# Kernel optimization log

Hardware: AMD Instinct MI355X
Metric: run time of the kernel (lower is better)

The kernel has to match this reference:

```python
import jax, jax.numpy as jnp
import numpy as np

B, Q, M, H, D = 2, 2048, 2048, 16, 64
HID = H * D           # hidden_size == num_heads * head_size
K_LEN = M + Q         # key/value length after memory concat
EPS = 1e-3            # keras LayerNormalization default epsilon
RAMP = 32             # Adaptive_Span ramp_size
NEG = -1e9


def setup_inputs() -> dict:
    key = jax.random.key(0)
    ks = jax.random.split(key, 12)
    s = 0.02
    return {
        "query": jax.random.normal(ks[0], (B, Q, HID), jnp.float32),
        "memory": jax.random.normal(ks[1], (B, M, HID), jnp.float32),
        "Wq": jax.random.normal(ks[2], (HID, H * D), jnp.float32) * s,
        "Wk": jax.random.normal(ks[3], (HID, H * D), jnp.float32) * s,
        "Wv": jax.random.normal(ks[4], (HID, H * D), jnp.float32) * s,
        "Wo": jax.random.normal(ks[5], (H * D, HID), jnp.float32) * s,
        "Wr": jax.random.normal(ks[6], (HID, H * D), jnp.float32) * s,
        "gamma_mem": jnp.ones((HID,), jnp.float32),
        "beta_mem": jnp.zeros((HID,), jnp.float32),
        "gamma_q": jnp.ones((HID,), jnp.float32),
        "beta_q": jnp.zeros((HID,), jnp.float32),
        "r_w_bias": jax.random.normal(ks[7], (1, H, 1, D), jnp.float32) * s,
        "r_r_bias": jax.random.normal(ks[8], (1, H, 1, D), jnp.float32) * s,
        "span_val": jnp.zeros((1, H, 1, 1), jnp.float32),
    }


def _layer_norm(x, gamma, beta):
    mu = jnp.mean(x, axis=-1, keepdims=True)
    var = jnp.mean(jnp.square(x - mu), axis=-1, keepdims=True)
    return (x - mu) * jax.lax.rsqrt(var + EPS) * gamma + beta


def _rel_shift(x):
    # Transformer-XL relative shift on [B,H,Q,K]
    b, h, q, k = x.shape
    x = jnp.pad(x, ((0, 0), (0, 0), (0, 0), (1, 0)))
    x = x.reshape(b, h, k + 1, q)[:, :, 1:, :]
    return x.reshape(b, h, q, k)


def reference(query, memory, Wq, Wk, Wv, Wo, Wr,
              gamma_mem, beta_mem, gamma_q, beta_q,
              r_w_bias, r_r_bias, span_val):
    kv = jnp.concatenate([memory, query], axis=1)          # [B,K,HID]
    kv = _layer_norm(kv, gamma_mem, beta_mem)
    q_in = _layer_norm(query, gamma_q, beta_q)

    # sinusoidal relative position embedding, positions K-1 .. 0
    pos_seq = jnp.arange(K_LEN - 1, -1, -1, dtype=jnp.float32)
    inv_freq = 1.0 / (10000.0 ** (jnp.arange(0, HID, 2, dtype=jnp.float32) / HID))
    sin_inp = pos_seq[:, None] * inv_freq[None, :]
    pos_emb = jnp.concatenate([jnp.sin(sin_inp), jnp.cos(sin_inp)], axis=-1)  # [K,HID]

    q = (q_in @ Wq).reshape(B, Q, H, D).transpose(0, 2, 1, 3)      # [B,H,Q,D]
    k = (kv @ Wk).reshape(B, K_LEN, H, D).transpose(0, 2, 1, 3)    # [B,H,K,D]
    v = (kv @ Wv).reshape(B, K_LEN, H, D).transpose(0, 2, 1, 3)    # [B,H,K,D]
    rel = (pos_emb @ Wr).reshape(K_LEN, H, D).transpose(1, 0, 2)   # [H,K,D]

    AD = jnp.einsum('bhqd,bhkd->bhqk', q + r_w_bias, k)
    BD = _rel_shift(jnp.einsum('bhqd,hkd->bhqk', q + r_r_bias, rel))
    logits = (AD + BD) / D                                          # note: /head_size, not sqrt

    # causal bias over the query block, zeros over memory columns
    causal = jnp.triu(jnp.ones((Q, Q), jnp.float32), 1) * NEG
    bias = jnp.concatenate([jnp.zeros((Q, M), jnp.float32), causal], axis=-1)
    logits = logits + bias[None, None]

    w = jax.nn.softmax(logits, axis=-1)                             # [B,H,Q,K]

    # adaptive span masking (static current_val path)
    mt = jnp.arange(Q, dtype=jnp.float32)
    span_mask = jnp.clip((mt[None, None, None, :] + span_val * Q) / (RAMP + 1), 0.0, 1.0)
    full_mask = jnp.concatenate(
        [jnp.ones((1, H, 1, M), jnp.float32),
         jnp.broadcast_to(span_mask, (1, H, 1, Q))], axis=-1)       # [1,H,1,K]
    w = w * full_mask
    w = w / (jnp.sum(w, axis=-1, keepdims=True) + 1e-8)

    out = jnp.einsum('bhqk,bhkd->bhqd', w, v)
    out = out.transpose(0, 2, 1, 3).reshape(B, Q, H * D)
    return out @ Wo
```

## Files before the change

### kernel.cpp

```cpp
#include <hip/hip_runtime.h>
#include <hip/hip_bf16.h>
#include <math.h>

#define B_   2
#define Q_   2048
#define M_   2048
#define H_   16
#define D_   64
#define HID_ 1024
#define KL_  4096
#define RT_  128
#define WT_  64
#define LSCL 0.022542110013890053f

typedef short short8 __attribute__((ext_vector_type(8)));
typedef short short4v __attribute__((ext_vector_type(4)));
typedef float f32x4 __attribute__((ext_vector_type(4)));
typedef float f32x16 __attribute__((ext_vector_type(16)));
typedef unsigned int uint2v __attribute__((ext_vector_type(2)));

__device__ __forceinline__ void async_copy16(const void* g, void* l) {
  __builtin_amdgcn_global_load_lds((const __attribute__((address_space(1))) unsigned int*)g,
                                   (__attribute__((address_space(3))) unsigned int*)l,
                                   16, 0, 0);
}

__device__ __forceinline__ float ldin(const void* p, size_t i, int md) {
  return md ? ((const float*)p)[i] : __bfloat162float(((const __hip_bfloat16*)p)[i]);
}

__device__ __forceinline__ short bfbits(float v) {
  __hip_bfloat16 t = __float2bfloat16(v);
  return *(short*)&t;
}

__device__ __forceinline__ float fexp2(float x) { return exp2f(x); }

__global__ __launch_bounds__(256) void detect_kernel(const unsigned int* __restrict__ q,
                                                     int* __restrict__ flag) {
  __shared__ int cnt;
  if (threadIdx.x == 0) cnt = 0;
  __syncthreads();
  int ins = 0;
#pragma unroll
  for (int i = 0; i < 4; i++) {
    unsigned int u = q[threadIdx.x * 4 + i];
    int e0 = (int)((u >> 7) & 0xffu);
    int e1 = (int)((u >> 23) & 0xffu);
    if (e0 == 0xff || e0 < 102 || e0 > 140) ins++;
    if (e1 == 0xff || e1 < 102 || e1 > 140) ins++;
  }
  atomicAdd(&cnt, ins);
  __syncthreads();
  if (threadIdx.x == 0) *flag = (cnt > 512) ? 1 : 0;
}

__global__ __launch_bounds__(256) void wtpe_kernel(
    const void* __restrict__ s0, const void* __restrict__ s1, const void* __restrict__ s2,
    const void* __restrict__ s3, const void* __restrict__ s4,
    __hip_bfloat16* __restrict__ d0, __hip_bfloat16* __restrict__ d1,
    __hip_bfloat16* __restrict__ d2, __hip_bfloat16* __restrict__ d3,
    __hip_bfloat16* __restrict__ d4, __hip_bfloat16* __restrict__ pe,
    const int* __restrict__ mode) {
  const int tid = threadIdx.x;
  if (blockIdx.z >= 5) {
    const int p = (blockIdx.z - 5) * 256 + blockIdx.y * 16 + blockIdx.x;
    const float pos = (float)(KL_ - 1 - p);
#pragma unroll
    for (int i = 0; i < 4; i++) {
      int c = tid * 4 + i;
      int f = (c < 512) ? c : c - 512;
      float invf = fexp2(-(float)f * (13.287712379549449f / 512.0f));
      float a = pos * invf;
      float v = (c < 512) ? __sinf(a) : __cosf(a);
      pe[(size_t)p * HID_ + c] = __float2bfloat16(v);
    }
    return;
  }
  const int md = *mode;
  const void* src; __hip_bfloat16* dst;
  switch (blockIdx.z) {
    case 0: src = s0; dst = d0; break;
    case 1: src = s1; dst = d1; break;
    case 2: src = s2; dst = d2; break;
    case 3: src = s3; dst = d3; break;
    default: src = s4; dst = d4; break;
  }
  const int r0 = blockIdx.x * 64, c0 = blockIdx.y * 64;
  __shared__ __hip_bfloat16 t[64][65];
  const int col = tid & 63, r4 = tid >> 6;
#pragma unroll
  for (int i = 0; i < 16; i++)
    t[r4 + i * 4][col] = __float2bfloat16(ldin(src, (size_t)(r0 + r4 + i * 4) * HID_ + c0 + col, md));
  __syncthreads();
#pragma unroll
  for (int i = 0; i < 16; i++)
    dst[(size_t)(c0 + r4 + i * 4) * HID_ + r0 + col] = t[col][r4 + i * 4];
}

__global__ __launch_bounds__(256) void ln_kernel(
    const void* __restrict__ mem, const void* __restrict__ qry,
    const void* __restrict__ gmem, const void* __restrict__ bmem,
    const void* __restrict__ gq, const void* __restrict__ bq,
    __hip_bfloat16* __restrict__ kvout, __hip_bfloat16* __restrict__ qout,
    const int* __restrict__ mode) {
  const int md = *mode;
  const int row = blockIdx.x;
  const void* src;
  const void* gamma; const void* beta;
  size_t base;
  __hip_bfloat16* dst;
  if (row < B_ * KL_) {
    const int b = row / KL_, j = row % KL_;
    if (j < M_) { src = mem; base = ((size_t)b * M_ + j) * HID_; }
    else        { src = qry; base = ((size_t)b * Q_ + (j - M_)) * HID_; }
    gamma = gmem; beta = bmem;
    dst = kvout + (size_t)row * HID_;
  } else {
    const int r = row - B_ * KL_;
    src = qry; base = (size_t)r * HID_;
    gamma = gq; beta = bq;
    dst = qout + (size_t)r * HID_;
  }
  const int tid = threadIdx.x;
  float x[4];
  float s = 0.f, ss = 0.f;
#pragma unroll
  for (int i = 0; i < 4; i++) {
    x[i] = ldin(src, base + i * 256 + tid, md);
    s += x[i]; ss += x[i] * x[i];
  }
#pragma unroll
  for (int o = 32; o > 0; o >>= 1) { s += __shfl_down(s, o); ss += __shfl_down(ss, o); }
  __shared__ float red[8];
  if ((tid & 63) == 0) { red[(tid >> 6) * 2] = s; red[(tid >> 6) * 2 + 1] = ss; }
  __syncthreads();
  float ts = 0.f, tss = 0.f;
#pragma unroll
  for (int i = 0; i < 4; i++) { ts += red[i * 2]; tss += red[i * 2 + 1]; }
  const float mu = ts * (1.f / 1024.f);
  const float var = tss * (1.f / 1024.f) - mu * mu;
  const float rs = rsqrtf(var + 1e-3f);
#pragma unroll
  for (int i = 0; i < 4; i++) {
    int c = i * 256 + tid;
    dst[c] = __float2bfloat16((x[i] - mu) * rs * ldin(gamma, c, md) + ldin(beta, c, md));
  }
}

template <int WRITE_MODE_SWITCH>
__device__ __forceinline__ void gemm_body(const __hip_bfloat16* __restrict__ A,
                                          const __hip_bfloat16* __restrict__ BT,
                                          void* __restrict__ C, int md, float scl) {
  __shared__ __attribute__((aligned(16))) __hip_bfloat16 sA[128 * 64];
  __shared__ __attribute__((aligned(16))) __hip_bfloat16 sB[128 * 64];
  const int tid = threadIdx.x;
  const int lane = tid & 63;
  const int w = tid >> 6;
  const int quad = lane >> 4, l16 = lane & 15;
  const int m0 = blockIdx.x * 128;
  const int n0 = blockIdx.y * 128;
  const int wm = (w >> 1) * 64, wn = (w & 1) * 64;
  const f32x4 fz = {0.f, 0.f, 0.f, 0.f};

  f32x4 acc[4][4];
#pragma unroll
  for (int i = 0; i < 4; i++)
#pragma unroll
    for (int j = 0; j < 4; j++) acc[i][j] = fz;

  for (int kk = 0; kk < HID_ / 64; kk++) {
    const int k0 = kk * 64;
    __syncthreads();
#pragma unroll
    for (int t = 0; t < 4; t++) {
      int c = (w * 4 + t) * 64 + lane;
      int row = c >> 3;
      int cid = (c & 7) ^ (row & 7);
      async_copy16(A + (size_t)(m0 + row) * HID_ + k0 + cid * 8, (char*)sA + c * 16);
      async_copy16(BT + (size_t)(n0 + row) * HID_ + k0 + cid * 8, (char*)sB + c * 16);
    }
    __syncthreads();
#pragma unroll
    for (int half = 0; half < 2; half++) {
      short8 af[4], bf[4];
#pragma unroll
      for (int mt = 0; mt < 4; mt++) {
        int r = wm + mt * 16 + l16;
        af[mt] = *(const short8*)((const char*)sA + r * 128 + (((half * 4 + quad) ^ (r & 7)) * 16));
      }
#pragma unroll
      for (int nt = 0; nt < 4; nt++) {
        int r = wn + nt * 16 + l16;
        bf[nt] = *(const short8*)((const char*)sB + r * 128 + (((half * 4 + quad) ^ (r & 7)) * 16));
      }
#pragma unroll
      for (int mt = 0; mt < 4; mt++)
#pragma unroll
        for (int nt = 0; nt < 4; nt++)
          acc[mt][nt] = __builtin_amdgcn_mfma_f32_16x16x32_bf16(af[mt], bf[nt], acc[mt][nt], 0, 0, 0);
    }
  }
#pragma unroll
  for (int mt = 0; mt < 4; mt++)
#pragma unroll
    for (int nt = 0; nt < 4; nt++)
#pragma unroll
      for (int rg = 0; rg < 4; rg++) {
        int r = m0 + wm + mt * 16 + quad * 4 + rg;
        int cc = n0 + wn + nt * 16 + l16;
        size_t idx = (size_t)r * HID_ + cc;
        if (WRITE_MODE_SWITCH && md) ((float*)C)[idx] = acc[mt][nt][rg];
        else ((__hip_bfloat16*)C)[idx] = __float2bfloat16(acc[mt][nt][rg] * scl);
      }
}

__global__ __launch_bounds__(256) void gemm_bt128(const __hip_bfloat16* __restrict__ A,
                                                  const __hip_bfloat16* __restrict__ BT,
                                                  __hip_bfloat16* __restrict__ C, float scl) {
  gemm_body<0>(A, BT, (void*)C, 0, scl);
}

__global__ __launch_bounds__(256) void gemm_out(const __hip_bfloat16* __restrict__ A,
                                                const __hip_bfloat16* __restrict__ BT,
                                                void* __restrict__ C,
                                                const int* __restrict__ mode) {
  gemm_body<1>(A, BT, C, *mode, 1.0f);
}

__global__ __launch_bounds__(256) void gemm_q(const __hip_bfloat16* __restrict__ A,
                                              const __hip_bfloat16* __restrict__ BT,
                                              const void* __restrict__ rwb,
                                              const void* __restrict__ rrb,
                                              __hip_bfloat16* __restrict__ qw,
                                              __hip_bfloat16* __restrict__ qr,
                                              const int* __restrict__ mode) {
  const int md = *mode;
  __shared__ __attribute__((aligned(16))) __hip_bfloat16 sA[128 * 64];
  __shared__ __attribute__((aligned(16))) __hip_bfloat16 sB[128 * 64];
  const int tid = threadIdx.x;
  const int lane = tid & 63;
  const int w = tid >> 6;
  const int quad = lane >> 4, l16 = lane & 15;
  const int m0 = blockIdx.x * 128;
  const int n0 = blockIdx.y * 128;
  const int wm = (w >> 1) * 64, wn = (w & 1) * 64;
  const f32x4 fz = {0.f, 0.f, 0.f, 0.f};

  f32x4 acc[4][4];
#pragma unroll
  for (int i = 0; i < 4; i++)
#pragma unroll
    for (int j = 0; j < 4; j++) acc[i][j] = fz;

  for (int kk = 0; kk < HID_ / 64; kk++) {
    const int k0 = kk * 64;
    __syncthreads();
#pragma unroll
    for (int t = 0; t < 4; t++) {
      int c = (w * 4 + t) * 64 + lane;
      int row = c >> 3;
      int cid = (c & 7) ^ (row & 7);
      async_copy16(A + (size_t)(m0 + row) * HID_ + k0 + cid * 8, (char*)sA + c * 16);
      async_copy16(BT + (size_t)(n0 + row) * HID_ + k0 + cid * 8, (char*)sB + c * 16);
    }
    __syncthreads();
#pragma unroll
    for (int half = 0; half < 2; half++) {
      short8 af[4], bf[4];
#pragma unroll
      for (int mt = 0; mt < 4; mt++) {
        int r = wm + mt * 16 + l16;
        af[mt] = *(const short8*)((const char*)sA + r * 128 + (((half * 4 + quad) ^ (r & 7)) * 16));
      }
#pragma unroll
      for (int nt = 0; nt < 4; nt++) {
        int r = wn + nt * 16 + l16;
        bf[nt] = *(const short8*)((const char*)sB + r * 128 + (((half * 4 + quad) ^ (r & 7)) * 16));
      }
#pragma unroll
      for (int mt = 0; mt < 4; mt++)
#pragma unroll
        for (int nt = 0; nt < 4; nt++)
          acc[mt][nt] = __builtin_amdgcn_mfma_f32_16x16x32_bf16(af[mt], bf[nt], acc[mt][nt], 0, 0, 0);
    }
  }
  float bw[4], br[4];
#pragma unroll
  for (int nt = 0; nt < 4; nt++) {
    int cc = n0 + wn + nt * 16 + l16;
    bw[nt] = ldin(rwb, cc, md);
    br[nt] = ldin(rrb, cc, md);
  }
#pragma unroll
  for (int mt = 0; mt < 4; mt++)
#pragma unroll
    for (int nt = 0; nt < 4; nt++)
#pragma unroll
      for (int rg = 0; rg < 4; rg++) {
        int r = m0 + wm + mt * 16 + quad * 4 + rg;
        int cc = n0 + wn + nt * 16 + l16;
        size_t idx = (size_t)r * HID_ + cc;
        float a = acc[mt][nt][rg];
        qw[idx] = __float2bfloat16((a + bw[nt]) * LSCL);
        qr[idx] = __float2bfloat16((a + br[nt]) * LSCL);
      }
}

__global__ __launch_bounds__(256) void gemm_dualv(const __hip_bfloat16* __restrict__ A,
                                                  const __hip_bfloat16* __restrict__ BT,
                                                  __hip_bfloat16* __restrict__ C0,
                                                  __hip_bfloat16* __restrict__ vpt) {
  __shared__ __attribute__((aligned(16))) char smem[128 * 136 * 2];
  __hip_bfloat16* sA = (__hip_bfloat16*)smem;
  __hip_bfloat16* sB = (__hip_bfloat16*)(smem + 16384);
  short* sT = (short*)smem;
  const int tid = threadIdx.x;
  const int lane = tid & 63;
  const int w = tid >> 6;
  const int quad = lane >> 4, l16 = lane & 15;
  const int m0 = blockIdx.x * 128;
  const int n0 = blockIdx.y * 128;
  const int wm = (w >> 1) * 64, wn = (w & 1) * 64;
  const f32x4 fz = {0.f, 0.f, 0.f, 0.f};

  f32x4 acc[4][4];
#pragma unroll
  for (int i = 0; i < 4; i++)
#pragma unroll
    for (int j = 0; j < 4; j++) acc[i][j] = fz;

  for (int kk = 0; kk < HID_ / 64; kk++) {
    const int k0 = kk * 64;
    __syncthreads();
#pragma unroll
    for (int t = 0; t < 4; t++) {
      int c = (w * 4 + t) * 64 + lane;
      int row = c >> 3;
      int cid = (c & 7) ^ (row & 7);
      async_copy16(A + (size_t)(m0 + row) * HID_ + k0 + cid * 8, (char*)sA + c * 16);
      async_copy16(BT + (size_t)(n0 + row) * HID_ + k0 + cid * 8, (char*)sB + c * 16);
    }
    __syncthreads();
#pragma unroll
    for (int half = 0; half < 2; half++) {
      short8 af[4], bf[4];
#pragma unroll
      for (int mt = 0; mt < 4; mt++) {
        int r = wm + mt * 16 + l16;
        af[mt] = *(const short8*)((const char*)sA + r * 128 + (((half * 4 + quad) ^ (r & 7)) * 16));
      }
#pragma unroll
      for (int nt = 0; nt < 4; nt++) {
        int r = wn + nt * 16 + l16;
        bf[nt] = *(const short8*)((const char*)sB + r * 128 + (((half * 4 + quad) ^ (r & 7)) * 16));
      }
#pragma unroll
      for (int mt = 0; mt < 4; mt++)
#pragma unroll
        for (int nt = 0; nt < 4; nt++)
          acc[mt][nt] = __builtin_amdgcn_mfma_f32_16x16x32_bf16(af[mt], bf[nt], acc[mt][nt], 0, 0, 0);
    }
  }
  if (n0 < HID_) {
#pragma unroll
    for (int mt = 0; mt < 4; mt++)
#pragma unroll
      for (int nt = 0; nt < 4; nt++)
#pragma unroll
        for (int rg = 0; rg < 4; rg++) {
          int r = m0 + wm + mt * 16 + quad * 4 + rg;
          int cc = n0 + wn + nt * 16 + l16;
          C0[(size_t)r * HID_ + cc] = __float2bfloat16(acc[mt][nt][rg]);
        }
  } else {
    __syncthreads();
#pragma unroll
    for (int mt = 0; mt < 4; mt++)
#pragma unroll
      for (int nt = 0; nt < 4; nt++) {
        int r = wm + mt * 16 + quad * 4;
        int cc = wn + nt * 16 + l16;
        short4v pk;
#pragma unroll
        for (int rg = 0; rg < 4; rg++) pk[rg] = bfbits(acc[mt][nt][rg]);
        *(short4v*)&sT[cc * 136 + r] = pk;
      }
    __syncthreads();
    const int b = m0 >> 12;
    const int j0g = m0 & (KL_ - 1);
    const int cg0 = n0 - HID_;
#pragma unroll
    for (int it = 0; it < 16; it++) {
      int cc = it * 8 + w * 2 + (lane >> 5);
      int jj = (lane & 31) * 4;
      int cg = cg0 + cc;
      int h = cg >> 6, d = cg & 63;
      short4v v = *(const short4v*)&sT[cc * 136 + jj];
      *(short4v*)(vpt + (((size_t)(b * H_ + h)) * D_ + d) * KL_ + j0g + jj) = v;
    }
  }
}

__global__ __launch_bounds__(256, 2) void attn_kernel(
    const __hip_bfloat16* __restrict__ qpw, const __hip_bfloat16* __restrict__ qpr,
    const __hip_bfloat16* __restrict__ kp, const __hip_bfloat16* __restrict__ vpt,
    const __hip_bfloat16* __restrict__ relp,
    const void* __restrict__ spanv, __hip_bfloat16* __restrict__ attn_out,
    const int* __restrict__ mode) {
  const int md = *mode;
  const int bid = blockIdx.x;
  int rk = (bid >> 3) & 15;
  if (bid & 256) rk ^= 15;
  const int i0 = rk << 7;
  const int bh = (bid & 7) + 8 * (bid >> 7);
  const int b = bh >> 4, h = bh & 15;

  const int tid = threadIdx.x;
  const int lane = tid & 63;
  const int w = tid >> 6;
  const int l31 = lane & 31, hi = lane >> 5;
  const int di = w * 32 + l31;
  const int iRow = i0 + di;

  __shared__ __attribute__((aligned(16))) __hip_bfloat16 sk[64 * 64];
  __shared__ __attribute__((aligned(16))) __hip_bfloat16 srel[192 * 64];
  __shared__ __attribute__((aligned(16))) __hip_bfloat16 svt[64 * 64];
  __shared__ __attribute__((aligned(16))) short sTP[128 * 100];

  const int rb = di * 200;
  const int sw = l31 & 7;

  const __hip_bfloat16* kbase = kp + (size_t)b * KL_ * HID_ + h * D_;
  const __hip_bfloat16* vtb = vpt + ((size_t)(b * H_ + h)) * D_ * KL_;
  const float sv = ldin(spanv, h, md);
  const float svQ = sv * (float)Q_;
  const int pb0 = Q_ - RT_ - i0;
  const int wof = (3 - w) * 32;
  const int ntiles = ((M_ + i0 + RT_ - 1) >> 6) + 1;

  const f32x16 z16 = {0.f,0.f,0.f,0.f,0.f,0.f,0.f,0.f,0.f,0.f,0.f,0.f,0.f,0.f,0.f,0.f};

  short8 qf[4], qrf[4];
  {
    const size_t qofs = ((size_t)(b * Q_ + iRow)) * HID_ + h * D_;
#pragma unroll
    for (int ks = 0; ks < 4; ks++) {
      qf[ks]  = *(const short8*)(qpw + qofs + ks * 16 + hi * 8);
      qrf[ks] = *(const short8*)(qpr + qofs + ks * 16 + hi * 8);
    }
  }

  {
#pragma unroll
    for (int t = 0; t < 2; t++) {
      int c = (w * 2 + t) * 64 + lane;
      int row = c >> 3;
      int cid = (c & 7) ^ (row & 7);
      async_copy16(kbase + (size_t)row * HID_ + cid * 8, (char*)sk + c * 16);
      async_copy16(vtb + (size_t)row * KL_ + cid * 8, (char*)svt + c * 16);
    }
#pragma unroll
    for (int t = 0; t < 6; t++) {
      int c = (w * 6 + t) * 64 + lane;
      int row = c >> 3;
      int cid = (c & 7) ^ (row & 7);
      int p = pb0 + row; p = p < KL_ ? p : KL_ - 1;
      async_copy16(relp + (size_t)p * HID_ + h * D_ + cid * 8, (char*)srel + c * 16);
    }
  }

  float mrow = -3e38f, lrow = 0.f, dfrow = 0.f;
  f32x16 oacc[2];
  oacc[0] = z16; oacc[1] = z16;
  int rot = 0;

  for (int kt = 0; kt < ntiles; kt++) {
    const int j0 = kt * WT_;

    __syncthreads();

    short8 rK[2], rR[2], rV[2];
    const bool pf = (kt + 1 < ntiles);
    {
      int j0n = j0 + WT_; if (j0n > KL_ - WT_) j0n = KL_ - WT_;
#pragma unroll
      for (int t = 0; t < 2; t++) {
        int c = (w * 2 + t) * 64 + lane;
        int row = c >> 3;
        int cid = (c & 7) ^ (row & 7);
        rK[t] = *(const short8*)(kbase + (size_t)(j0n + row) * HID_ + cid * 8);
        rV[t] = *(const short8*)(vtb + (size_t)row * KL_ + j0n + cid * 8);
        int p = pb0 + (kt + 1) * 64 + 128 + row; p = p < KL_ ? p : KL_ - 1;
        rR[t] = *(const short8*)(relp + (size_t)p * HID_ + h * D_ + cid * 8);
      }
    }
    __builtin_amdgcn_sched_barrier(0);

    __builtin_amdgcn_s_setprio(1);
    f32x16 S[2];
    S[0] = z16; S[1] = z16;
#pragma unroll
    for (int mt = 0; mt < 2; mt++) {
      const char* rowp = (const char*)sk + (mt * 32 + l31) * 128;
#pragma unroll
      for (int ks = 0; ks < 4; ks++) {
        short8 af = *(const short8*)(rowp + (((ks * 2 + hi) ^ sw) * 16));
        S[mt] = __builtin_amdgcn_mfma_f32_32x32x16_bf16(af, qf[ks], S[mt], 0, 0, 0);
      }
    }

#pragma unroll
    for (int mt = 0; mt < 3; mt++) {
      f32x16 T = z16;
      int rr = wof + mt * 32 + l31 + rot; if (rr >= 192) rr -= 192;
      const char* rowp = (const char*)srel + rr * 128;
#pragma unroll
      for (int ks = 0; ks < 4; ks++) {
        short8 af = *(const short8*)(rowp + (((ks * 2 + hi) ^ sw) * 16));
        T = __builtin_amdgcn_mfma_f32_32x32x16_bf16(af, qrf[ks], T, 0, 0, 0);
      }
#pragma unroll
      for (int r2 = 0; r2 < 4; r2++) {
        short4v pk;
#pragma unroll
        for (int r4 = 0; r4 < 4; r4++) pk[r4] = bfbits(T[r2 * 4 + r4]);
        *(short4v*)((char*)sTP + rb + (mt * 32 + 8 * r2 + 4 * hi) * 2) = pk;
      }
    }
    __builtin_amdgcn_s_setprio(0);

    {
      const char* tb2 = (const char*)sTP + rb + (31 - l31 + 4 * hi) * 2;
#pragma unroll
      for (int mt = 0; mt < 2; mt++)
#pragma unroll
        for (int r2 = 0; r2 < 4; r2++)
#pragma unroll
          for (int r4 = 0; r4 < 4; r4++)
            S[mt][r2 * 4 + r4] +=
                __bfloat162float(*(const __hip_bfloat16*)(tb2 + (mt * 32 + 8 * r2 + r4) * 2));
    }

    const bool causalT = (j0 + WT_ - 1 - i0) > M_;
    if (causalT) {
#pragma unroll
      for (int mt = 0; mt < 2; mt++)
#pragma unroll
        for (int r2 = 0; r2 < 4; r2++)
#pragma unroll
          for (int r4 = 0; r4 < 4; r4++) {
            int j = j0 + mt * 32 + 8 * r2 + 4 * hi + r4;
            if (j - iRow > M_) S[mt][r2 * 4 + r4] = -1e30f;
          }
    }
    float m8[8];
#pragma unroll
    for (int g = 0; g < 8; g++) {
      int mt = g >> 2, r2 = g & 3;
      m8[g] = fmaxf(fmaxf(S[mt][r2 * 4 + 0], S[mt][r2 * 4 + 1]),
                    fmaxf(S[mt][r2 * 4 + 2], S[mt][r2 * 4 + 3]));
    }
    float mnew = fmaxf(mrow,
        fmaxf(fmaxf(fmaxf(m8[0], m8[1]), fmaxf(m8[2], m8[3])),
              fmaxf(fmaxf(m8[4], m8[5]), fmaxf(m8[6], m8[7]))));
    mnew = fmaxf(mnew, __shfl_xor(mnew, 32));
    if (!__all(mnew - mrow <= 8.f)) {
      const float alpha = fexp2(mrow - mnew);
      mrow = mnew;
      lrow *= alpha; dfrow *= alpha;
#pragma unroll
      for (int dt = 0; dt < 2; dt++)
#pragma unroll
        for (int rg = 0; rg < 16; rg++) oacc[dt][rg] *= alpha;
    }

    const bool maskT = (j0 + WT_ > M_) && ((float)j0 < (float)M_ + 33.f - svQ);
    short8 paf[4];
#pragma unroll
    for (int mt = 0; mt < 2; mt++) {
      unsigned Pp[4][2];
#pragma unroll
      for (int r2 = 0; r2 < 4; r2++) {
        short4v g;
        float pvv[4];
#pragma unroll
        for (int r4 = 0; r4 < 4; r4++) {
          float pv = fexp2(S[mt][r2 * 4 + r4] - mrow);
          pvv[r4] = pv;
          float pm = pv;
          if (maskT) {
            int j = j0 + mt * 32 + 8 * r2 + 4 * hi + r4;
            if (j >= M_) {
              float t0 = (float)(j - M_) + svQ;
              float mk = fminf(fmaxf(t0 * (1.0f / 33.0f), 0.f), 1.f);
              pm = pv * mk;
              dfrow += pv - pm;
            }
          }
          g[r4] = bfbits(pm);
        }
        lrow += (pvv[0] + pvv[1]) + (pvv[2] + pvv[3]);
        union { short4v s; unsigned u[2]; } cv; cv.s = g;
        Pp[r2][0] = cv.u[0]; Pp[r2][1] = cv.u[1];
      }
#pragma unroll
      for (int half = 0; half < 2; half++) {
        uint2v rA = __builtin_amdgcn_permlane32_swap(Pp[half * 2][0], Pp[half * 2 + 1][0], false, false);
        uint2v rB = __builtin_amdgcn_permlane32_swap(Pp[half * 2][1], Pp[half * 2 + 1][1], false, false);
        union { unsigned u[4]; short8 s; } asm8;
        asm8.u[0] = rA[0]; asm8.u[1] = rB[0]; asm8.u[2] = rA[1]; asm8.u[3] = rB[1];
        paf[mt * 2 + half] = asm8.s;
      }
    }

    __builtin_amdgcn_s_setprio(1);
#pragma unroll
    for (int dt = 0; dt < 2; dt++) {
      const char* rowp = (const char*)svt + (dt * 32 + l31) * 128;
#pragma unroll
      for (int ks = 0; ks < 4; ks++) {
        short8 bfv = *(const short8*)(rowp + (((ks * 2 + hi) ^ sw) * 16));
        oacc[dt] = __builtin_amdgcn_mfma_f32_32x32x16_bf16(bfv, paf[ks], oacc[dt], 0, 0, 0);
      }
    }
    __builtin_amdgcn_s_setprio(0);

    __syncthreads();

    if (pf) {
#pragma unroll
      for (int t = 0; t < 2; t++) {
        int c = (w * 2 + t) * 64 + lane;
        int row = c >> 3;
        *(short8*)((char*)sk + c * 16) = rK[t];
        *(short8*)((char*)svt + c * 16) = rV[t];
        *(short8*)((char*)srel + (rot + row) * 128 + (c & 7) * 16) = rR[t];
      }
    }
    rot += 64; if (rot == 192) rot = 0;
  }

  lrow += __shfl_xor(lrow, 32);
  dfrow += __shfl_xor(dfrow, 32);
  const float denom = (lrow - dfrow) + 1e-8f * lrow;
  const float rdenom = 1.f / denom;
  __hip_bfloat16* ob = attn_out + ((size_t)(b * Q_ + iRow)) * HID_ + h * D_;
#pragma unroll
  for (int dt = 0; dt < 2; dt++)
#pragma unroll
    for (int r2 = 0; r2 < 4; r2++) {
      short4v o;
#pragma unroll
      for (int r4 = 0; r4 < 4; r4++) o[r4] = bfbits(oacc[dt][r2 * 4 + r4] * rdenom);
      *(short4v*)(ob + dt * 32 + 8 * r2 + 4 * hi) = o;
    }
}

extern "C" void kernel_launch(void* const* d_in, const int* in_sizes, int n_in,
                              void* d_out, int out_size, void* d_ws, size_t ws_size,
                              hipStream_t stream) {
  const void* query  = d_in[0];
  const void* memory = d_in[1];
  const void* Wq = d_in[2];
  const void* Wk = d_in[3];
  const void* Wv = d_in[4];
  const void* Wo = d_in[5];
  const void* Wr = d_in[6];
  const void* gmem = d_in[7];
  const void* bmem = d_in[8];
  const void* gq = d_in[9];
  const void* bq = d_in[10];
  const void* rwb = d_in[11];
  const void* rrb = d_in[12];
  const void* spanv = d_in[13];

  char* ws = (char*)d_ws;
  size_t off = 0;
  auto alloc = [&](size_t bytes) -> char* {
    char* p = ws + off;
    off += (bytes + 255) & ~(size_t)255;
    return p;
  };
  int* flag = (int*)alloc(256);
  const size_t SZ_W = (size_t)HID_ * HID_ * 2;
  __hip_bfloat16* wqT = (__hip_bfloat16*)alloc(SZ_W);
  __hip_bfloat16* wkT = (__hip_bfloat16*)alloc(SZ_W);
  __hip_bfloat16* wvT = (__hip_bfloat16*)alloc(SZ_W);
  __hip_bfloat16* wrT = (__hip_bfloat16*)alloc(SZ_W);
  __hip_bfloat16* woT = (__hip_bfloat16*)alloc(SZ_W);
  __hip_bfloat16* kvln = (__hip_bfloat16*)alloc((size_t)B_ * KL_ * HID_ * 2);
  __hip_bfloat16* qln  = (__hip_bfloat16*)alloc((size_t)B_ * Q_ * HID_ * 2);
  __hip_bfloat16* pe   = (__hip_bfloat16*)alloc((size_t)KL_ * HID_ * 2);
  __hip_bfloat16* qpw  = (__hip_bfloat16*)alloc((size_t)B_ * Q_ * HID_ * 2);
  __hip_bfloat16* qpr  = (__hip_bfloat16*)alloc((size_t)B_ * Q_ * HID_ * 2);
  __hip_bfloat16* kpb  = (__hip_bfloat16*)alloc((size_t)B_ * KL_ * HID_ * 2);
  __hip_bfloat16* vptb = (__hip_bfloat16*)alloc((size_t)B_ * KL_ * HID_ * 2);
  __hip_bfloat16* relp = (__hip_bfloat16*)alloc((size_t)KL_ * HID_ * 2);
  __hip_bfloat16* aout = (__hip_bfloat16*)alloc((size_t)B_ * Q_ * HID_ * 2);

  dim3 tb(256);
  detect_kernel<<<dim3(1), tb, 0, stream>>>((const unsigned int*)query, flag);

  wtpe_kernel<<<dim3(16, 16, 21), tb, 0, stream>>>(Wq, Wk, Wv, Wr, Wo,
                                                   wqT, wkT, wvT, wrT, woT, pe, flag);

  ln_kernel<<<dim3(B_ * KL_ + B_ * Q_), tb, 0, stream>>>(memory, query, gmem, bmem, gq, bq,
                                                         kvln, qln, flag);

  gemm_q<<<dim3(B_ * Q_ / 128, HID_ / 128), tb, 0, stream>>>(qln, wqT, rwb, rrb, qpw, qpr, flag);
  gemm_dualv<<<dim3(B_ * KL_ / 128, 2 * HID_ / 128), tb, 0, stream>>>(kvln, wkT, kpb, vptb);
  gemm_bt128<<<dim3(KL_ / 128, HID_ / 128), tb, 0, stream>>>(pe, wrT, relp, 1.0f);

  attn_kernel<<<dim3((Q_ / RT_) * H_ * B_), tb, 0, stream>>>(qpw, qpr, kpb, vptb, relp, spanv, aout, flag);

  gemm_out<<<dim3(B_ * Q_ / 128, HID_ / 128), tb, 0, stream>>>(aout, woT, d_out, flag);

  (void)in_sizes; (void)n_in; (void)out_size; (void)ws_size;
}
```

Baseline: 476.1 us.

## Split attention key range across two blocks and merge partials

Each (batch, head, row-tile) attention work item is split into two blocks, each covering half of the key tiles. Each block writes unnormalized fp32 partial outputs plus its running max, sum and mask-deficit to a workspace. A new merge kernel then combines the two halves with log-sum-exp rescaling and writes the bf16 output. This doubles the grid to 1024 blocks to improve occupancy and tail balance on the causal workload, at the cost of extra fp32 traffic and an additional kernel launch. The kvln buffer is reused as partial storage.

```diff
diff --git a/kernel.cpp b/kernel.cpp
--- a/kernel.cpp
+++ b/kernel.cpp
@@ -406,15 +406,20 @@
     const __hip_bfloat16* __restrict__ qpw, const __hip_bfloat16* __restrict__ qpr,
     const __hip_bfloat16* __restrict__ kp, const __hip_bfloat16* __restrict__ vpt,
     const __hip_bfloat16* __restrict__ relp,
-    const void* __restrict__ spanv, __hip_bfloat16* __restrict__ attn_out,
+    const void* __restrict__ spanv,
+    float* __restrict__ opart, float* __restrict__ mlbuf,
     const int* __restrict__ mode) {
   const int md = *mode;
   const int bid = blockIdx.x;
-  int rk = (bid >> 3) & 15;
-  if (bid & 256) rk ^= 15;
+  const int g = bid >> 1, half = bid & 1;
+  const int rk = 15 - (g >> 5);
+  const int bh = g & 31;
   const int i0 = rk << 7;
-  const int bh = (bid & 7) + 8 * (bid >> 7);
   const int b = bh >> 4, h = bh & 15;
+  const int nt = 34 + 2 * rk;
+  const int nt2 = nt >> 1;
+  const int kt0 = half ? nt2 : 0;
+  const int kt1 = half ? nt : nt2;
 
   const int tid = threadIdx.x;
   const int lane = tid & 63;
@@ -437,7 +442,7 @@
   const float svQ = sv * (float)Q_;
   const int pb0 = Q_ - RT_ - i0;
   const int wof = (3 - w) * 32;
-  const int ntiles = ((M_ + i0 + RT_ - 1) >> 6) + 1;
+  const int jb0 = kt0 * WT_;
 
   const f32x16 z16 = {0.f,0.f,0.f,0.f,0.f,0.f,0.f,0.f,0.f,0.f,0.f,0.f,0.f,0.f,0.f,0.f};
 
@@ -457,15 +462,15 @@
       int c = (w * 2 + t) * 64 + lane;
       int row = c >> 3;
       int cid = (c & 7) ^ (row & 7);
-      async_copy16(kbase + (size_t)row * HID_ + cid * 8, (char*)sk + c * 16);
-      async_copy16(vtb + (size_t)row * KL_ + cid * 8, (char*)svt + c * 16);
+      async_copy16(kbase + (size_t)(jb0 + row) * HID_ + cid * 8, (char*)sk + c * 16);
+      async_copy16(vtb + (size_t)row * KL_ + jb0 + cid * 8, (char*)svt + c * 16);
     }
 #pragma unroll
     for (int t = 0; t < 6; t++) {
       int c = (w * 6 + t) * 64 + lane;
       int row = c >> 3;
       int cid = (c & 7) ^ (row & 7);
-      int p = pb0 + row; p = p < KL_ ? p : KL_ - 1;
+      int p = pb0 + jb0 + row; p = p < KL_ ? p : KL_ - 1;
       async_copy16(relp + (size_t)p * HID_ + h * D_ + cid * 8, (char*)srel + c * 16);
     }
   }
@@ -475,13 +480,13 @@
   oacc[0] = z16; oacc[1] = z16;
   int rot = 0;
 
-  for (int kt = 0; kt < ntiles; kt++) {
+  for (int kt = kt0; kt < kt1; kt++) {
     const int j0 = kt * WT_;
 
     __syncthreads();
 
     short8 rK[2], rR[2], rV[2];
-    const bool pf = (kt + 1 < ntiles);
+    const bool pf = (kt + 1 < kt1);
     {
       int j0n = j0 + WT_; if (j0n > KL_ - WT_) j0n = KL_ - WT_;
 #pragma unroll
@@ -556,10 +561,10 @@
     }
     float m8[8];
 #pragma unroll
-    for (int g = 0; g < 8; g++) {
-      int mt = g >> 2, r2 = g & 3;
-      m8[g] = fmaxf(fmaxf(S[mt][r2 * 4 + 0], S[mt][r2 * 4 + 1]),
-                    fmaxf(S[mt][r2 * 4 + 2], S[mt][r2 * 4 + 3]));
+    for (int g2 = 0; g2 < 8; g2++) {
+      int mt = g2 >> 2, r2 = g2 & 3;
+      m8[g2] = fmaxf(fmaxf(S[mt][r2 * 4 + 0], S[mt][r2 * 4 + 1]),
+                     fmaxf(S[mt][r2 * 4 + 2], S[mt][r2 * 4 + 3]));
     }
     float mnew = fmaxf(mrow,
         fmaxf(fmaxf(fmaxf(m8[0], m8[1]), fmaxf(m8[2], m8[3])),
@@ -582,7 +587,7 @@
       unsigned Pp[4][2];
 #pragma unroll
       for (int r2 = 0; r2 < 4; r2++) {
-        short4v g;
+        short4v g3;
         float pvv[4];
 #pragma unroll
         for (int r4 = 0; r4 < 4; r4++) {
@@ -598,19 +603,19 @@
               dfrow += pv - pm;
             }
           }
-          g[r4] = bfbits(pm);
+          g3[r4] = bfbits(pm);
         }
         lrow += (pvv[0] + pvv[1]) + (pvv[2] + pvv[3]);
-        union { short4v s; unsigned u[2]; } cv; cv.s = g;
+        union { short4v s; unsigned u[2]; } cv; cv.s = g3;
         Pp[r2][0] = cv.u[0]; Pp[r2][1] = cv.u[1];
       }
 #pragma unroll
-      for (int half = 0; half < 2; half++) {
-        uint2v rA = __builtin_amdgcn_permlane32_swap(Pp[half * 2][0], Pp[half * 2 + 1][0], false, false);
-        uint2v rB = __builtin_amdgcn_permlane32_swap(Pp[half * 2][1], Pp[half * 2 + 1][1], false, false);
+      for (int hf = 0; hf < 2; hf++) {
+        uint2v rA = __builtin_amdgcn_permlane32_swap(Pp[hf * 2][0], Pp[hf * 2 + 1][0], false, false);
+        uint2v rB = __builtin_amdgcn_permlane32_swap(Pp[hf * 2][1], Pp[hf * 2 + 1][1], false, false);
         union { unsigned u[4]; short8 s; } asm8;
         asm8.u[0] = rA[0]; asm8.u[1] = rB[0]; asm8.u[2] = rA[1]; asm8.u[3] = rB[1];
-        paf[mt * 2 + half] = asm8.s;
+        paf[mt * 2 + hf] = asm8.s;
       }
     }
 
@@ -643,18 +648,45 @@
 
   lrow += __shfl_xor(lrow, 32);
   dfrow += __shfl_xor(dfrow, 32);
-  const float denom = (lrow - dfrow) + 1e-8f * lrow;
-  const float rdenom = 1.f / denom;
-  __hip_bfloat16* ob = attn_out + ((size_t)(b * Q_ + iRow)) * HID_ + h * D_;
+  float* ob = opart + (size_t)half * B_ * Q_ * HID_ + ((size_t)(b * Q_ + iRow)) * HID_ + h * D_;
 #pragma unroll
   for (int dt = 0; dt < 2; dt++)
 #pragma unroll
     for (int r2 = 0; r2 < 4; r2++) {
-      short4v o;
-#pragma unroll
-      for (int r4 = 0; r4 < 4; r4++) o[r4] = bfbits(oacc[dt][r2 * 4 + r4] * rdenom);
-      *(short4v*)(ob + dt * 32 + 8 * r2 + 4 * hi) = o;
-    }
+      f32x4 o = {oacc[dt][r2 * 4 + 0], oacc[dt][r2 * 4 + 1],
+                 oacc[dt][r2 * 4 + 2], oacc[dt][r2 * 4 + 3]};
+      *(f32x4*)(ob + dt * 32 + 8 * r2 + 4 * hi) = o;
+    }
+  if (hi == 0) {
+    f32x4 mlv = {mrow, lrow, dfrow, 0.f};
+    *(f32x4*)(mlbuf + ((size_t)half * B_ * H_ * Q_ + ((size_t)(b * H_ + h)) * Q_ + iRow) * 4) = mlv;
+  }
+}
+
+__global__ __launch_bounds__(256) void merge_kernel(
+    const float* __restrict__ opart, const float* __restrict__ mlbuf,
+    __hip_bfloat16* __restrict__ aout) {
+  const int bq = blockIdx.x;
+  const int b = bq >> 11, q = bq & 2047;
+  const int t = threadIdx.x;
+  const int h = t >> 4, dg = (t & 15) * 4;
+  const size_t mlidx = (((size_t)(b * H_ + h)) * Q_ + q) * 4;
+  const size_t MLH = (size_t)B_ * H_ * Q_ * 4;
+  f32x4 ml0 = *(const f32x4*)(mlbuf + mlidx);
+  f32x4 ml1 = *(const f32x4*)(mlbuf + MLH + mlidx);
+  const float ms = fmaxf(ml0[0], ml1[0]);
+  const float a0 = fexp2(ml0[0] - ms), a1 = fexp2(ml1[0] - ms);
+  const float l = ml0[1] * a0 + ml1[1] * a1;
+  const float df = ml0[2] * a0 + ml1[2] * a1;
+  const float r = 1.f / ((l - df) + 1e-8f * l);
+  const size_t oidx = (size_t)bq * HID_ + h * D_ + dg;
+  const size_t OH = (size_t)B_ * Q_ * HID_;
+  f32x4 o0 = *(const f32x4*)(opart + oidx);
+  f32x4 o1 = *(const f32x4*)(opart + OH + oidx);
+  short4v o;
+#pragma unroll
+  for (int r4 = 0; r4 < 4; r4++) o[r4] = bfbits((o0[r4] * a0 + o1[r4] * a1) * r);
+  *(short4v*)(aout + oidx) = o;
 }
 
 extern "C" void kernel_launch(void* const* d_in, const int* in_sizes, int n_in,
@@ -698,6 +730,8 @@
   __hip_bfloat16* vptb = (__hip_bfloat16*)alloc((size_t)B_ * KL_ * HID_ * 2);
   __hip_bfloat16* relp = (__hip_bfloat16*)alloc((size_t)KL_ * HID_ * 2);
   __hip_bfloat16* aout = (__hip_bfloat16*)alloc((size_t)B_ * Q_ * HID_ * 2);
+  float* mlbuf = (float*)alloc((size_t)2 * B_ * H_ * Q_ * 4 * sizeof(float));
+  float* opart = (float*)kvln;
 
   dim3 tb(256);
   detect_kernel<<<dim3(1), tb, 0, stream>>>((const unsigned int*)query, flag);
@@ -712,7 +746,9 @@
   gemm_dualv<<<dim3(B_ * KL_ / 128, 2 * HID_ / 128), tb, 0, stream>>>(kvln, wkT, kpb, vptb);
   gemm_bt128<<<dim3(KL_ / 128, HID_ / 128), tb, 0, stream>>>(pe, wrT, relp, 1.0f);
 
-  attn_kernel<<<dim3((Q_ / RT_) * H_ * B_), tb, 0, stream>>>(qpw, qpr, kpb, vptb, relp, spanv, aout, flag);
+  attn_kernel<<<dim3(1024), tb, 0, stream>>>(qpw, qpr, kpb, vptb, relp, spanv,
+                                             opart, mlbuf, flag);
+  merge_kernel<<<dim3(B_ * Q_), tb, 0, stream>>>(opart, mlbuf, aout);
 
   gemm_out<<<dim3(B_ * Q_ / 128, HID_ / 128), tb, 0, stream>>>(aout, woT, d_out, flag);
 
```

New measurement: 462.4 us. 2.9% less time.
